# Optimization experiments

Measured on AMD Instinct MI355X. Metric: run time of the kernel, lower is better.

The kernel has to match this reference:

```python
import jax, jax.numpy as jnp
import numpy as np

B, N = 2, 200
IMG = 2048
NC = 4                    # node concepts ('Is*')
NODE_CH = NC * 256        # 1024
EC = 3                    # edge concepts minus 'HigherPri'
AC = 4                    # actions
BBOX_MAX = 1024.0
E = N * (N - 1)

# static fully-connected directed edge list (src=i, dst=j, i!=j), row-major order
_ii, _jj = np.meshgrid(np.arange(N), np.arange(N), indexing='ij')
_m = _ii != _jj
SRC = jnp.asarray(_ii[_m])
DST = jnp.asarray(_jj[_m])


def _lin(k, fin, fout):
    kw, kb = jax.random.split(k)
    s = 1.0 / np.sqrt(fin)
    return (jax.random.uniform(kw, (fin, fout), jnp.float32, -s, s),
            jax.random.uniform(kb, (fout,), jnp.float32, -s, s))


def setup_inputs():
    ks = jax.random.split(jax.random.key(0), 16)
    p = {}
    p['roi_features'] = jax.random.normal(ks[0], (B, N, IMG), jnp.float32)
    p['batch_bboxes'] = jax.random.uniform(ks[1], (B, N, 4), jnp.float32) * BBOX_MAX
    p['batch_directions'] = jax.random.normal(ks[2], (B, N, 4), jnp.float32)
    p['batch_priorities'] = jax.random.normal(ks[3], (B, N), jnp.float32)
    p['w1'], p['b1'] = _lin(ks[4], IMG, 512)
    p['w2'], p['b2'] = _lin(ks[5], 512, 256)
    p['w3'], p['b3'] = _lin(ks[6], 256, NODE_CH)
    p['wi'], p['bi'] = _lin(ks[7], NODE_CH, NC)
    p['we1'], p['be1'] = _lin(ks[8], 16, 256)
    p['we2'], p['be2'] = _lin(ks[9], 256, 64)
    p['we3'], p['be3'] = _lin(ks[10], 64, EC)
    p['wp1'], p['bp1'] = _lin(ks[11], EC + 1, 128)
    p['wp2'], p['bp2'] = _lin(ks[12], 128, NODE_CH * AC)
    p['root_w'], _ = _lin(ks[13], NODE_CH, AC)
    _, p['root_b'] = _lin(ks[14], NODE_CH, AC)
    return p


def reference(roi_features, batch_bboxes, batch_directions, batch_priorities,
              w1, b1, w2, b2, w3, b3, wi, bi,
              we1, be1, we2, be2, we3, be3,
              wp1, bp1, wp2, bp2, root_w, root_b):
    # node concept embedding MLP: [B,N,IMG] -> [B,N,NODE_CH]
    h = jax.nn.relu(roi_features @ w1 + b1)
    h = jax.nn.relu(h @ w2 + b2)
    node_concepts = h @ w3 + b3
    node_concepts_explicit = jax.nn.sigmoid(node_concepts @ wi + bi)

    # pairwise attributes for all directed edges (same ordering as torch masks)
    node_attr = jnp.concatenate([batch_bboxes / BBOX_MAX, batch_directions], -1)  # [B,N,8]
    pair = jnp.concatenate([node_attr[:, SRC], node_attr[:, DST]], -1)            # [B,E,16]
    eh = jax.nn.relu(pair @ we1 + be1)
    eh = jax.nn.relu(eh @ we2 + be2)
    edge_attributes = jax.nn.sigmoid(eh @ we3 + be3)                              # [B,E,EC]
    higher_pri = (batch_priorities[:, SRC] > batch_priorities[:, DST]).astype(jnp.float32)
    edge_attributes = jnp.concatenate([edge_attributes, higher_pri[..., None]], -1)  # [B,E,EC+1]

    # NNConv on graph 0: per-edge weight matrix, gather-matmul-scatter
    x = node_concepts[0]                 # [N, NODE_CH]
    e = edge_attributes[0]               # [E, EC+1]
    w = jax.nn.relu(e @ wp1 + bp1) @ wp2 + bp2
    w = w.reshape(E, NODE_CH, AC)        # [E, NODE_CH, AC]
    msg = jnp.einsum('ei,eio->eo', x[SRC], w)          # [E, AC]
    agg = jax.ops.segment_sum(msg, DST, num_segments=N)  # [N, AC]
    next_actions = agg + x @ root_w + root_b
    return (next_actions, node_concepts_explicit[0], edge_attributes[0])
```

## Files before the change

kernel.cpp:

```cpp
#include <hip/hip_runtime.h>
#include <math.h>

#define NN 200
#define ETOT 39800

typedef float float4v __attribute__((ext_vector_type(4)));
typedef short short8 __attribute__((ext_vector_type(8)));
typedef unsigned int uint4v __attribute__((ext_vector_type(4)));

__device__ __forceinline__ float sigf(float x) { return 1.0f / (1.0f + expf(-x)); }

__device__ __forceinline__ unsigned short f2b(float f) {
  unsigned u = __float_as_uint(f);
  u += 0x7fffu + ((u >> 16) & 1u);
  return (unsigned short)(u >> 16);
}
__device__ __forceinline__ unsigned pk2(float a, float b) {
  unsigned r;
  asm("v_cvt_pk_bf16_f32 %0, %1, %2" : "=v"(r) : "v"(a), "v"(b));
  return r;
}
__device__ __forceinline__ float4v mfma16(short8 a, short8 b, float4v c) {
  return __builtin_amdgcn_mfma_f32_16x16x32_bf16(a, b, c, 0, 0, 0);
}

union SharedU {
  float trans[64][65];
  float red[4][16][34];
  struct { int src_s[64]; int dst_s[64]; } e;
};

template <int KSTEPS>
__device__ __forceinline__ float tile_core(const unsigned short* __restrict__ A,
                                           const unsigned short* __restrict__ B,
                                           int m0, int n0, int K, float (&red)[4][16][34]) {
  const int tid = threadIdx.x, lane = tid & 63, wv = tid >> 6;
  const int mr = lane & 15, quad = lane >> 4;
  const unsigned short* Ap = A + (size_t)(m0 + mr) * K + wv * (KSTEPS * 32) + quad * 8;
  const unsigned short* Bp = B + (size_t)(n0 + mr) * K + wv * (KSTEPS * 32) + quad * 8;
  float4v acc0 = {0.f, 0.f, 0.f, 0.f}, acc1 = {0.f, 0.f, 0.f, 0.f};
#pragma unroll
  for (int s = 0; s < KSTEPS; s += 2) {
    acc0 = mfma16(*(const short8*)(Ap + s * 32), *(const short8*)(Bp + s * 32), acc0);
    acc1 = mfma16(*(const short8*)(Ap + (s + 1) * 32), *(const short8*)(Bp + (s + 1) * 32), acc1);
  }
  float4v acc = acc0 + acc1;
#pragma unroll
  for (int r = 0; r < 4; ++r) red[wv][quad * 4 + r][mr] = acc[r];
  __syncthreads();
  const int row = tid >> 4, col = tid & 15;
  return red[0][row][col] + red[1][row][col] + red[2][row][col] + red[3][row][col];
}

template <int KSTEPS>
__device__ __forceinline__ void tile_core2(const unsigned short* __restrict__ A,
                                           const unsigned short* __restrict__ B,
                                           int m0, int n0, int K,
                                           float& v0, float& v1, float (&red)[4][16][34]) {
  const int tid = threadIdx.x, lane = tid & 63, wv = tid >> 6;
  const int mr = lane & 15, quad = lane >> 4;
  const unsigned short* Ap = A + (size_t)(m0 + mr) * K + wv * (KSTEPS * 32) + quad * 8;
  const unsigned short* B0 = B + (size_t)(n0 + mr) * K + wv * (KSTEPS * 32) + quad * 8;
  const unsigned short* B1 = B0 + (size_t)16 * K;
  float4v a0 = {0.f, 0.f, 0.f, 0.f}, a1 = {0.f, 0.f, 0.f, 0.f};
#pragma unroll
  for (int s = 0; s < KSTEPS; ++s) {
    short8 af = *(const short8*)(Ap + s * 32);
    a0 = mfma16(af, *(const short8*)(B0 + s * 32), a0);
    a1 = mfma16(af, *(const short8*)(B1 + s * 32), a1);
  }
#pragma unroll
  for (int r = 0; r < 4; ++r) {
    red[wv][quad * 4 + r][mr] = a0[r];
    red[wv][quad * 4 + r][17 + mr] = a1[r];
  }
  __syncthreads();
  const int row = tid >> 4, col = tid & 15;
  v0 = red[0][row][col] + red[1][row][col] + red[2][row][col] + red[3][row][col];
  v1 = red[0][row][17 + col] + red[1][row][17 + col] + red[2][row][17 + col] + red[3][row][17 + col];
}

__global__ __launch_bounds__(256) void k_prep(
    const float* __restrict__ w1, const float* __restrict__ roi,
    const float* __restrict__ bbox, const float* __restrict__ dir,
    const float* __restrict__ we1, const float* __restrict__ be1,
    const float* __restrict__ we2,
    unsigned short* __restrict__ w1T, unsigned short* __restrict__ roiB,
    float* __restrict__ P, float* __restrict__ Q, unsigned short* __restrict__ we2T) {
  __shared__ float lds[64][65];
  const int b = blockIdx.x, tid = threadIdx.x;
  if (b < 256) {
    const int kt = b % 32, nt = b / 32;
#pragma unroll 4
    for (int i = 0; i < 16; ++i) {
      int idx = tid + i * 256, r = idx >> 6, c = idx & 63;
      lds[r][c] = w1[(size_t)(kt * 64 + r) * 512 + nt * 64 + c];
    }
    __syncthreads();
#pragma unroll 4
    for (int i = 0; i < 16; ++i) {
      int idx = tid + i * 256, r = idx >> 6, c = idx & 63;
      w1T[(size_t)(nt * 64 + r) * 2048 + kt * 64 + c] = f2b(lds[c][r]);
    }
  } else if (b < 456) {
    int n = b - 256;
    const float4v* R4 = (const float4v*)(roi + (size_t)n * 2048);
    unsigned long long* O = (unsigned long long*)(roiB + (size_t)n * 2048);
#pragma unroll
    for (int j = 0; j < 2; ++j) {
      int idx = tid + j * 256;
      float4v v = R4[idx];
      union { unsigned u[2]; unsigned long long ll; } pk;
      pk.u[0] = pk2(v[0], v[1]);
      pk.u[1] = pk2(v[2], v[3]);
      O[idx] = pk.ll;
    }
  } else if (b < 656) {
    int n = b - 456, c = tid;
    float aa[8];
#pragma unroll
    for (int r = 0; r < 4; ++r) aa[r] = bbox[n * 4 + r] * (1.0f / 1024.0f);
#pragma unroll
    for (int r = 0; r < 4; ++r) aa[4 + r] = dir[n * 4 + r];
    float p = be1[c], q = 0.0f;
#pragma unroll
    for (int r = 0; r < 8; ++r) {
      p += aa[r] * we1[r * 256 + c];
      q += aa[r] * we1[(8 + r) * 256 + c];
    }
    P[n * 256 + c] = p;
    Q[n * 256 + c] = q;
  } else {
    int f = (b - 656) * 256 + tid;
    int c = f >> 6, k0 = (f & 63) * 4;
#pragma unroll
    for (int q = 0; q < 4; ++q)
      we2T[c * 256 + k0 + q] = f2b(we2[(k0 + q) * 64 + c]);
  }
}

__global__ __launch_bounds__(256) void k_g1x(
    const unsigned short* __restrict__ roiB, const unsigned short* __restrict__ w1T,
    const float* __restrict__ b1, unsigned short* __restrict__ h1,
    const float* __restrict__ P, const float* __restrict__ Q,
    const unsigned short* __restrict__ we2T,
    const float* __restrict__ be2, const float* __restrict__ we3, const float* __restrict__ be3,
    const float* __restrict__ pri, float* __restrict__ out_ea,
    const float* __restrict__ w2, unsigned short* __restrict__ w2T,
    const float* __restrict__ wp2, const float* __restrict__ wi,
    const float* __restrict__ rootw, const float* __restrict__ bp2,
    unsigned short* __restrict__ Ac,
    const float* __restrict__ w3, const float* __restrict__ b3, unsigned short* __restrict__ Bc,
    const float* __restrict__ wp1, float* __restrict__ wp1T) {
  __shared__ SharedU sh;
  const int t = blockIdx.x, tid = threadIdx.x;
  if (t < 416) {
    const int m0 = (t % 13) * 16, n0 = (t / 13) * 16;
    float v = tile_core<16>(roiB, w1T, m0, n0, 2048, sh.red);
    const int row = tid >> 4, col = tid & 15;
    v += b1[n0 + col];
    v = fmaxf(v, 0.f);
    h1[(size_t)(m0 + row) * 512 + n0 + col] = f2b(v);
  } else if (t < 1038) {
    const int e0 = (t - 416) * 64;
    if (tid < 64) {
      int e = e0 + tid;
      int i = -1, j = 0;
      if (e < ETOT) {
        i = e / 199;
        int jj = e - i * 199;
        j = jj + (jj >= i ? 1 : 0);
      }
      sh.e.src_s[tid] = i;
      sh.e.dst_s[tid] = j;
    }
    __syncthreads();

    const int lane = tid & 63;
    const int wv = tid >> 6;
    const int m = lane & 15;
    const int quad = lane >> 4;
    const int eloc = wv * 16 + m;
    const int si = sh.e.src_s[eloc];
    const int dj = sh.e.dst_s[eloc];

    float4v acc[4];
#pragma unroll
    for (int ct = 0; ct < 4; ++ct) { acc[ct][0] = 0.f; acc[ct][1] = 0.f; acc[ct][2] = 0.f; acc[ct][3] = 0.f; }

    const short8* W8 = (const short8*)we2T;

    for (int ks = 0; ks < 8; ++ks) {
      union { short8 s; uint4v u; } af;
      af.s = (short8)0;
      if (si >= 0) {
        const float4v* p4 = (const float4v*)(P + si * 256 + ks * 32 + quad * 8);
        const float4v* q4 = (const float4v*)(Q + dj * 256 + ks * 32 + quad * 8);
        float4v v0 = p4[0] + q4[0];
        float4v v1 = p4[1] + q4[1];
        af.u[0] = pk2(fmaxf(v0[0], 0.f), fmaxf(v0[1], 0.f));
        af.u[1] = pk2(fmaxf(v0[2], 0.f), fmaxf(v0[3], 0.f));
        af.u[2] = pk2(fmaxf(v1[0], 0.f), fmaxf(v1[1], 0.f));
        af.u[3] = pk2(fmaxf(v1[2], 0.f), fmaxf(v1[3], 0.f));
      }
#pragma unroll
      for (int ct = 0; ct < 4; ++ct) {
        short8 bf = W8[(ct * 16 + m) * 32 + ks * 4 + quad];
        acc[ct] = __builtin_amdgcn_mfma_f32_16x16x32_bf16(af.s, bf, acc[ct], 0, 0, 0);
      }
    }

    float ev[4][3];
#pragma unroll
    for (int r = 0; r < 4; ++r) { ev[r][0] = 0.f; ev[r][1] = 0.f; ev[r][2] = 0.f; }
#pragma unroll
    for (int ct = 0; ct < 4; ++ct) {
      const int col = ct * 16 + m;
      const float b2v = be2[col];
      const float w0 = we3[col * 3 + 0], w1v = we3[col * 3 + 1], w2v = we3[col * 3 + 2];
#pragma unroll
      for (int r = 0; r < 4; ++r) {
        float e2 = fmaxf(acc[ct][r] + b2v, 0.f);
        ev[r][0] += e2 * w0;
        ev[r][1] += e2 * w1v;
        ev[r][2] += e2 * w2v;
      }
    }
#pragma unroll
    for (int r = 0; r < 4; ++r)
#pragma unroll
      for (int p = 0; p < 3; ++p) {
        float v = ev[r][p];
        v += __shfl_xor(v, 1, 64);
        v += __shfl_xor(v, 2, 64);
        v += __shfl_xor(v, 4, 64);
        v += __shfl_xor(v, 8, 64);
        ev[r][p] = v;
      }
    if (m == 0) {
#pragma unroll
      for (int r = 0; r < 4; ++r) {
        int el = wv * 16 + quad * 4 + r;
        int ss = sh.e.src_s[el], dd = sh.e.dst_s[el];
        if (ss >= 0) {
          float4v o;
          o[0] = sigf(ev[r][0] + be3[0]);
          o[1] = sigf(ev[r][1] + be3[1]);
          o[2] = sigf(ev[r][2] + be3[2]);
          o[3] = (pri[ss] > pri[dd]) ? 1.0f : 0.0f;
          *(float4v*)(out_ea + (size_t)(e0 + el) * 4) = o;
        }
      }
    }
  } else if (t < 1070) {
    const int tt = t - 1038, kt = tt % 8, nt = tt / 8;
#pragma unroll 4
    for (int i = 0; i < 16; ++i) {
      int idx = tid + i * 256, r = idx >> 6, c = idx & 63;
      sh.trans[r][c] = w2[(size_t)(kt * 64 + r) * 256 + nt * 64 + c];
    }
    __syncthreads();
#pragma unroll 4
    for (int i = 0; i < 16; ++i) {
      int idx = tid + i * 256, r = idx >> 6, c = idx & 63;
      w2T[(size_t)(nt * 64 + r) * 512 + kt * 64 + c] = f2b(sh.trans[c][r]);
    }
  } else if (t < 1198) {
    int k = t - 1070;
    int o = tid >> 6, l = tid & 63;
    const float* src = wp2 + (size_t)k * 4096;
    unsigned short* dst = Ac + (size_t)(k * 4 + o) * 1024;
    for (int i = l; i < 1024; i += 64) dst[i] = f2b(src[i * 4 + o]);
  } else if (t < 1214) {
    int r = t - 1198;
    unsigned short* dst = Ac + (size_t)(512 + r) * 1024;
    const float* src = (r < 4) ? (wi + r) : (r < 8) ? (rootw + (r - 4))
                     : (r < 12) ? (bp2 + (r - 8)) : nullptr;
    for (int i = tid; i < 1024; i += 256)
      dst[i] = src ? f2b(src[i * 4]) : (unsigned short)0;
  } else if (t < 1286) {
    int rb = (t - 1214) * 4;
#pragma unroll
    for (int j = 0; j < 16; ++j) {
      int idx = tid + j * 256;
      int row = rb + (idx >> 10), i = idx & 1023;
      float val = (row < 256) ? w3[(size_t)row * 1024 + i] : (row == 256 ? b3[i] : 0.0f);
      Bc[(size_t)row * 1024 + i] = f2b(val);
    }
  } else {
    if (tid < 128) {
      float4v v = {wp1[tid], wp1[128 + tid], wp1[256 + tid], wp1[384 + tid]};
      ((float4v*)wp1T)[tid] = v;
    }
  }
}

__global__ __launch_bounds__(256) void k_g2x(
    const unsigned short* __restrict__ h1, const unsigned short* __restrict__ w2T,
    const float* __restrict__ b2, unsigned short* __restrict__ h2,
    const unsigned short* __restrict__ Ac, const unsigned short* __restrict__ Bc,
    unsigned short* __restrict__ CT, float* __restrict__ biasT) {
  __shared__ SharedU sh;
  const int t = blockIdx.x, tid = threadIdx.x;
  if (t < 208) {
    const int m0 = (t % 13) * 16, n0 = (t / 13) * 16;
    float v = tile_core<4>(h1, w2T, m0, n0, 512, sh.red);
    const int row = tid >> 4, col = tid & 15;
    v += b2[n0 + col];
    v = fmaxf(v, 0.f);
    h2[(size_t)(m0 + row) * 256 + n0 + col] = f2b(v);
  } else {
    const int u = t - 208, mi = u % 33, nj = u / 33;
    const int m0 = mi * 16, n0 = nj * 32;
    float v0, v1;
    tile_core2<8>(Ac, Bc, m0, n0, 1024, v0, v1, sh.red);
    const int row = tid >> 4, col = tid & 15;
    const int m = m0 + row;
    const int c0 = n0 + col, c1 = n0 + 16 + col;
    if (c0 < 256) CT[(size_t)m * 256 + c0] = f2b(v0);
    else if (c0 == 256) biasT[m] = v0;
    if (c1 < 256) CT[(size_t)m * 256 + c1] = f2b(v1);
  }
}

__global__ __launch_bounds__(256) void k_tfused(const unsigned short* __restrict__ h2,
                                                const unsigned short* __restrict__ CT,
                                                const float* __restrict__ biasT,
                                                const float* __restrict__ bi,
                                                const float* __restrict__ rootb,
                                                float* __restrict__ Tm, float* __restrict__ out1,
                                                float* __restrict__ out0, float* __restrict__ U) {
  __shared__ SharedU sh;
  const int m0 = blockIdx.x * 16, n0 = blockIdx.y * 16, tid = threadIdx.x;
  float v = tile_core<2>(h2, CT, m0, n0, 256, sh.red);
  const int row = tid >> 4, col = tid & 15;
  const int n = m0 + row, c = n0 + col;
  v += biasT[c];
  if (c < 512) {
    Tm[(size_t)n * 512 + c] = v;
  } else if (n < NN) {
    int r = c - 512;
    if (r < 4) out1[n * 4 + r] = sigf(v + bi[r]);
    else if (r < 8) out0[n * 4 + (r - 4)] = v + rootb[r - 4];
    else if (r < 12) U[n * 4 + (r - 8)] = v;
  }
}

__global__ __launch_bounds__(256) void k_tail(
    const float* __restrict__ ea, const float* __restrict__ wp1T, const float* __restrict__ bp1,
    const float* __restrict__ T, const float* __restrict__ U,
    float* __restrict__ out0) {
  __shared__ int src_s[64], dst_s[64];
  __shared__ float4v ea_s[64];
  __shared__ float4v wp1s[128];
  __shared__ float bp1s[128];
  __shared__ float4v Ts[2][128];
  __shared__ float Us[2][4];

  const int tid = threadIdx.x;
  const int e0 = blockIdx.x * 64;
  const int s_lo = e0 / 199;

  if (tid < 64) {
    int e = e0 + tid;
    int i = -1, j = 0;
    if (e < ETOT) {
      i = e / 199;
      int jj = e - i * 199;
      j = jj + (jj >= i ? 1 : 0);
      ea_s[tid] = ((const float4v*)ea)[e];
    }
    src_s[tid] = i;
    dst_s[tid] = j;
  }
  if (tid < 128) {
    wp1s[tid] = ((const float4v*)wp1T)[tid];
    bp1s[tid] = bp1[tid];
  }
  {
    int row = tid >> 7, c = tid & 127;
    Ts[row][c] = ((const float4v*)T)[(s_lo + row) * 128 + c];
  }
  if (tid < 8) {
    int s = min(s_lo + (tid >> 2), 199);
    Us[tid >> 2][tid & 3] = U[s * 4 + (tid & 3)];
  }
  __syncthreads();

  const int ee = tid >> 2, pp = tid & 3;
  const int s2 = src_s[ee], d2 = dst_s[ee];
  float4v pm = {0.f, 0.f, 0.f, 0.f};
  if (s2 >= 0) {
    const int srow = s2 - s_lo;
    const float4v c4 = ea_s[ee];
    const float c0 = c4[0], c1 = c4[1], c2 = c4[2], c3 = c4[3];
#pragma unroll 8
    for (int tt = pp; tt < 128; tt += 4) {
      float4v w4 = wp1s[tt];
      float hv = bp1s[tt] + c0 * w4[0] + c1 * w4[1] + c2 * w4[2] + c3 * w4[3];
      hv = fmaxf(hv, 0.f);
      pm += hv * Ts[srow][tt];
    }
  }
#pragma unroll
  for (int o = 0; o < 4; ++o) {
    float v = pm[o];
    v += __shfl_xor(v, 1, 64);
    v += __shfl_xor(v, 2, 64);
    pm[o] = v;
  }
  if (s2 >= 0) atomicAdd(&out0[d2 * 4 + pp], Us[s2 - s_lo][pp] + pm[pp]);
}

extern "C" void kernel_launch(void* const* d_in, const int* in_sizes, int n_in,
                              void* d_out, int out_size, void* d_ws, size_t ws_size,
                              hipStream_t stream) {
  (void)in_sizes; (void)n_in; (void)out_size; (void)ws_size;
  const float* roi   = (const float*)d_in[0];
  const float* bbox  = (const float*)d_in[1];
  const float* dir   = (const float*)d_in[2];
  const float* pri   = (const float*)d_in[3];
  const float* w1    = (const float*)d_in[4];
  const float* b1    = (const float*)d_in[5];
  const float* w2    = (const float*)d_in[6];
  const float* b2    = (const float*)d_in[7];
  const float* w3    = (const float*)d_in[8];
  const float* b3    = (const float*)d_in[9];
  const float* wi    = (const float*)d_in[10];
  const float* bi    = (const float*)d_in[11];
  const float* we1   = (const float*)d_in[12];
  const float* be1   = (const float*)d_in[13];
  const float* we2   = (const float*)d_in[14];
  const float* be2   = (const float*)d_in[15];
  const float* we3   = (const float*)d_in[16];
  const float* be3   = (const float*)d_in[17];
  const float* wp1   = (const float*)d_in[18];
  const float* bp1   = (const float*)d_in[19];
  const float* wp2   = (const float*)d_in[20];
  const float* bp2   = (const float*)d_in[21];
  const float* rootw = (const float*)d_in[22];
  const float* rootb = (const float*)d_in[23];

  float* out0 = (float*)d_out;
  float* out1 = out0 + 800;
  float* out2 = out0 + 1600;

  unsigned short* us = (unsigned short*)d_ws;
  unsigned short* w1T  = us;
  unsigned short* w2T  = us + 1048576;
  unsigned short* Ac   = us + 1179648;
  unsigned short* Bc   = us + 1720320;
  unsigned short* we2T = us + 2015232;
  unsigned short* roiB = us + 2031616;
  unsigned short* h1   = us + 2457600;
  unsigned short* h2   = us + 2564096;
  unsigned short* CT   = us + 2617344;
  float* fb    = (float*)(us + 2752512);
  float* Tm    = fb;
  float* Pm    = fb + 106496;
  float* Qm    = fb + 157696;
  float* Um    = fb + 208896;
  float* wp1Tp = fb + 209696;
  float* biasT = fb + 210208;

  k_prep<<<672, 256, 0, stream>>>(w1, roi, bbox, dir, we1, be1, we2,
                                  w1T, roiB, Pm, Qm, we2T);

  k_g1x<<<1287, 256, 0, stream>>>(roiB, w1T, b1, h1,
                                  Pm, Qm, we2T, be2, we3, be3, pri, out2,
                                  w2, w2T,
                                  wp2, wi, rootw, bp2, Ac,
                                  w3, b3, Bc,
                                  wp1, wp1Tp);

  k_g2x<<<505, 256, 0, stream>>>(h1, w2T, b2, h2, Ac, Bc, CT, biasT);

  k_tfused<<<dim3(13, 33), 256, 0, stream>>>(h2, CT, biasT, bi, rootb, Tm, out1, out0, Um);

  k_tail<<<622, 256, 0, stream>>>(out2, wp1Tp, bp1, Tm, Um, out0);
}
```

Before: 155.2 us.

## Fuse layer-2 GEMM, transform GEMM and edge tail into per-node final kernel

Moves all weight-conversion work into the prep kernel and runs the Ac·Bc product in the same launch as the layer-1 GEMM and the edge MLP. The layer-2 matmul, the projection through CT and the per-edge message aggregation are merged into one kernel with one block per source node. Each block computes its node's h2 and T rows in LDS with scalar FMAs instead of MFMA, then processes that node's 199 outgoing edges. This cuts the pipeline from five launches to three and removes the global round trips for h2, T and U, at the cost of scalar fp32 math and only 200 blocks in the last stage.

```diff
diff --git a/kernel.cpp b/kernel.cpp
--- a/kernel.cpp
+++ b/kernel.cpp
@@ -15,6 +15,11 @@
   u += 0x7fffu + ((u >> 16) & 1u);
   return (unsigned short)(u >> 16);
 }
+__device__ __forceinline__ float b2f16(unsigned short u) {
+  return __uint_as_float(((unsigned)u) << 16);
+}
+__device__ __forceinline__ float blo(unsigned u) { return __uint_as_float(u << 16); }
+__device__ __forceinline__ float bhi(unsigned u) { return __uint_as_float(u & 0xffff0000u); }
 __device__ __forceinline__ unsigned pk2(float a, float b) {
   unsigned r;
   asm("v_cvt_pk_bf16_f32 %0, %1, %2" : "=v"(r) : "v"(a), "v"(b));
@@ -84,9 +89,15 @@
     const float* __restrict__ w1, const float* __restrict__ roi,
     const float* __restrict__ bbox, const float* __restrict__ dir,
     const float* __restrict__ we1, const float* __restrict__ be1,
-    const float* __restrict__ we2,
+    const float* __restrict__ we2, const float* __restrict__ w2,
+    const float* __restrict__ wp2, const float* __restrict__ wi,
+    const float* __restrict__ rootw, const float* __restrict__ bp2,
+    const float* __restrict__ w3, const float* __restrict__ b3,
+    const float* __restrict__ wp1,
     unsigned short* __restrict__ w1T, unsigned short* __restrict__ roiB,
-    float* __restrict__ P, float* __restrict__ Q, unsigned short* __restrict__ we2T) {
+    float* __restrict__ P, float* __restrict__ Q, unsigned short* __restrict__ we2T,
+    unsigned short* __restrict__ w2T, unsigned short* __restrict__ Ac,
+    unsigned short* __restrict__ Bc, float* __restrict__ wp1T) {
   __shared__ float lds[64][65];
   const int b = blockIdx.x, tid = threadIdx.x;
   if (b < 256) {
@@ -130,28 +141,64 @@
     }
     P[n * 256 + c] = p;
     Q[n * 256 + c] = q;
-  } else {
+  } else if (b < 672) {
     int f = (b - 656) * 256 + tid;
     int c = f >> 6, k0 = (f & 63) * 4;
 #pragma unroll
     for (int q = 0; q < 4; ++q)
       we2T[c * 256 + k0 + q] = f2b(we2[(k0 + q) * 64 + c]);
-  }
-}
-
-__global__ __launch_bounds__(256) void k_g1x(
+  } else if (b < 704) {
+    const int tt = b - 672, kt = tt % 8, nt = tt / 8;
+#pragma unroll 4
+    for (int i = 0; i < 16; ++i) {
+      int idx = tid + i * 256, r = idx >> 6, c = idx & 63;
+      lds[r][c] = w2[(size_t)(kt * 64 + r) * 256 + nt * 64 + c];
+    }
+    __syncthreads();
+#pragma unroll 4
+    for (int i = 0; i < 16; ++i) {
+      int idx = tid + i * 256, r = idx >> 6, c = idx & 63;
+      w2T[(size_t)(nt * 64 + r) * 512 + kt * 64 + c] = f2b(lds[c][r]);
+    }
+  } else if (b < 832) {
+    int k = b - 704;
+    int o = tid >> 6, l = tid & 63;
+    const float* src = wp2 + (size_t)k * 4096;
+    unsigned short* dst = Ac + (size_t)(k * 4 + o) * 1024;
+    for (int i = l; i < 1024; i += 64) dst[i] = f2b(src[i * 4 + o]);
+  } else if (b < 848) {
+    int r = b - 832;
+    unsigned short* dst = Ac + (size_t)(512 + r) * 1024;
+    const float* src = (r < 4) ? (wi + r) : (r < 8) ? (rootw + (r - 4))
+                     : (r < 12) ? (bp2 + (r - 8)) : nullptr;
+    for (int i = tid; i < 1024; i += 256)
+      dst[i] = src ? f2b(src[i * 4]) : (unsigned short)0;
+  } else if (b < 920) {
+    int rb = (b - 848) * 4;
+#pragma unroll
+    for (int j = 0; j < 16; ++j) {
+      int idx = tid + j * 256;
+      int row = rb + (idx >> 10), i = idx & 1023;
+      float val = (row < 256) ? w3[(size_t)row * 1024 + i] : (row == 256 ? b3[i] : 0.0f);
+      Bc[(size_t)row * 1024 + i] = f2b(val);
+    }
+  } else {
+    if (tid < 128) {
+      float4v v = {wp1[tid], wp1[128 + tid], wp1[256 + tid], wp1[384 + tid]};
+      ((float4v*)wp1T)[tid] = v;
+    }
+  }
+}
+
+__global__ __launch_bounds__(256) void k_main(
     const unsigned short* __restrict__ roiB, const unsigned short* __restrict__ w1T,
     const float* __restrict__ b1, unsigned short* __restrict__ h1,
     const float* __restrict__ P, const float* __restrict__ Q,
     const unsigned short* __restrict__ we2T,
     const float* __restrict__ be2, const float* __restrict__ we3, const float* __restrict__ be3,
     const float* __restrict__ pri, float* __restrict__ out_ea,
-    const float* __restrict__ w2, unsigned short* __restrict__ w2T,
-    const float* __restrict__ wp2, const float* __restrict__ wi,
-    const float* __restrict__ rootw, const float* __restrict__ bp2,
-    unsigned short* __restrict__ Ac,
-    const float* __restrict__ w3, const float* __restrict__ b3, unsigned short* __restrict__ Bc,
-    const float* __restrict__ wp1, float* __restrict__ wp1T) {
+    const unsigned short* __restrict__ Ac, const unsigned short* __restrict__ Bc,
+    unsigned short* __restrict__ CT, float* __restrict__ biasT) {
   __shared__ SharedU sh;
   const int t = blockIdx.x, tid = threadIdx.x;
   if (t < 416) {
@@ -252,65 +299,8 @@
         }
       }
     }
-  } else if (t < 1070) {
-    const int tt = t - 1038, kt = tt % 8, nt = tt / 8;
-#pragma unroll 4
-    for (int i = 0; i < 16; ++i) {
-      int idx = tid + i * 256, r = idx >> 6, c = idx & 63;
-      sh.trans[r][c] = w2[(size_t)(kt * 64 + r) * 256 + nt * 64 + c];
-    }
-    __syncthreads();
-#pragma unroll 4
-    for (int i = 0; i < 16; ++i) {
-      int idx = tid + i * 256, r = idx >> 6, c = idx & 63;
-      w2T[(size_t)(nt * 64 + r) * 512 + kt * 64 + c] = f2b(sh.trans[c][r]);
-    }
-  } else if (t < 1198) {
-    int k = t - 1070;
-    int o = tid >> 6, l = tid & 63;
-    const float* src = wp2 + (size_t)k * 4096;
-    unsigned short* dst = Ac + (size_t)(k * 4 + o) * 1024;
-    for (int i = l; i < 1024; i += 64) dst[i] = f2b(src[i * 4 + o]);
-  } else if (t < 1214) {
-    int r = t - 1198;
-    unsigned short* dst = Ac + (size_t)(512 + r) * 1024;
-    const float* src = (r < 4) ? (wi + r) : (r < 8) ? (rootw + (r - 4))
-                     : (r < 12) ? (bp2 + (r - 8)) : nullptr;
-    for (int i = tid; i < 1024; i += 256)
-      dst[i] = src ? f2b(src[i * 4]) : (unsigned short)0;
-  } else if (t < 1286) {
-    int rb = (t - 1214) * 4;
-#pragma unroll
-    for (int j = 0; j < 16; ++j) {
-      int idx = tid + j * 256;
-      int row = rb + (idx >> 10), i = idx & 1023;
-      float val = (row < 256) ? w3[(size_t)row * 1024 + i] : (row == 256 ? b3[i] : 0.0f);
-      Bc[(size_t)row * 1024 + i] = f2b(val);
-    }
   } else {
-    if (tid < 128) {
-      float4v v = {wp1[tid], wp1[128 + tid], wp1[256 + tid], wp1[384 + tid]};
-      ((float4v*)wp1T)[tid] = v;
-    }
-  }
-}
-
-__global__ __launch_bounds__(256) void k_g2x(
-    const unsigned short* __restrict__ h1, const unsigned short* __restrict__ w2T,
-    const float* __restrict__ b2, unsigned short* __restrict__ h2,
-    const unsigned short* __restrict__ Ac, const unsigned short* __restrict__ Bc,
-    unsigned short* __restrict__ CT, float* __restrict__ biasT) {
-  __shared__ SharedU sh;
-  const int t = blockIdx.x, tid = threadIdx.x;
-  if (t < 208) {
-    const int m0 = (t % 13) * 16, n0 = (t / 13) * 16;
-    float v = tile_core<4>(h1, w2T, m0, n0, 512, sh.red);
-    const int row = tid >> 4, col = tid & 15;
-    v += b2[n0 + col];
-    v = fmaxf(v, 0.f);
-    h2[(size_t)(m0 + row) * 256 + n0 + col] = f2b(v);
-  } else {
-    const int u = t - 208, mi = u % 33, nj = u / 33;
+    const int u = t - 1038, mi = u % 33, nj = u / 33;
     const int m0 = mi * 16, n0 = nj * 32;
     float v0, v1;
     tile_core2<8>(Ac, Bc, m0, n0, 1024, v0, v1, sh.red);
@@ -323,93 +313,100 @@
   }
 }
 
-__global__ __launch_bounds__(256) void k_tfused(const unsigned short* __restrict__ h2,
-                                                const unsigned short* __restrict__ CT,
-                                                const float* __restrict__ biasT,
-                                                const float* __restrict__ bi,
-                                                const float* __restrict__ rootb,
-                                                float* __restrict__ Tm, float* __restrict__ out1,
-                                                float* __restrict__ out0, float* __restrict__ U) {
-  __shared__ SharedU sh;
-  const int m0 = blockIdx.x * 16, n0 = blockIdx.y * 16, tid = threadIdx.x;
-  float v = tile_core<2>(h2, CT, m0, n0, 256, sh.red);
-  const int row = tid >> 4, col = tid & 15;
-  const int n = m0 + row, c = n0 + col;
-  v += biasT[c];
-  if (c < 512) {
-    Tm[(size_t)n * 512 + c] = v;
-  } else if (n < NN) {
-    int r = c - 512;
-    if (r < 4) out1[n * 4 + r] = sigf(v + bi[r]);
-    else if (r < 8) out0[n * 4 + (r - 4)] = v + rootb[r - 4];
-    else if (r < 12) U[n * 4 + (r - 8)] = v;
-  }
-}
-
-__global__ __launch_bounds__(256) void k_tail(
-    const float* __restrict__ ea, const float* __restrict__ wp1T, const float* __restrict__ bp1,
-    const float* __restrict__ T, const float* __restrict__ U,
-    float* __restrict__ out0) {
-  __shared__ int src_s[64], dst_s[64];
-  __shared__ float4v ea_s[64];
+__global__ __launch_bounds__(256) void k_final(
+    const unsigned short* __restrict__ h1, const unsigned short* __restrict__ w2T,
+    const float* __restrict__ b2,
+    const unsigned short* __restrict__ CT, const float* __restrict__ biasT,
+    const float* __restrict__ bi, const float* __restrict__ rootb,
+    const float* __restrict__ ea,
+    const float* __restrict__ wp1T, const float* __restrict__ bp1,
+    float* __restrict__ out0, float* __restrict__ out1) {
+  __shared__ float h1s[512];
+  __shared__ float h2f[256];
+  __shared__ float4v Ts4[128];
   __shared__ float4v wp1s[128];
   __shared__ float bp1s[128];
-  __shared__ float4v Ts[2][128];
-  __shared__ float Us[2][4];
-
-  const int tid = threadIdx.x;
-  const int e0 = blockIdx.x * 64;
-  const int s_lo = e0 / 199;
-
-  if (tid < 64) {
-    int e = e0 + tid;
-    int i = -1, j = 0;
-    if (e < ETOT) {
-      i = e / 199;
-      int jj = e - i * 199;
-      j = jj + (jj >= i ? 1 : 0);
-      ea_s[tid] = ((const float4v*)ea)[e];
-    }
-    src_s[tid] = i;
-    dst_s[tid] = j;
+  __shared__ float Us[4];
+  const int s = blockIdx.x, tid = threadIdx.x;
+
+  {
+    unsigned u = ((const unsigned*)(h1 + (size_t)s * 512))[tid];
+    h1s[2 * tid] = blo(u);
+    h1s[2 * tid + 1] = bhi(u);
   }
   if (tid < 128) {
     wp1s[tid] = ((const float4v*)wp1T)[tid];
     bp1s[tid] = bp1[tid];
   }
+  __syncthreads();
+
   {
-    int row = tid >> 7, c = tid & 127;
-    Ts[row][c] = ((const float4v*)T)[(s_lo + row) * 128 + c];
-  }
-  if (tid < 8) {
-    int s = min(s_lo + (tid >> 2), 199);
-    Us[tid >> 2][tid & 3] = U[s * 4 + (tid & 3)];
+    const uint4v* W4 = (const uint4v*)(w2T + (size_t)tid * 512);
+    float acc = b2[tid];
+#pragma unroll 8
+    for (int j = 0; j < 64; ++j) {
+      uint4v w = W4[j];
+      const float4v* hp = (const float4v*)&h1s[j * 8];
+      float4v ha = hp[0], hb = hp[1];
+      acc += ha[0] * blo(w[0]) + ha[1] * bhi(w[0]) + ha[2] * blo(w[1]) + ha[3] * bhi(w[1]) +
+             hb[0] * blo(w[2]) + hb[1] * bhi(w[2]) + hb[2] * blo(w[3]) + hb[3] * bhi(w[3]);
+    }
+    h2f[tid] = fmaxf(acc, 0.f);
   }
   __syncthreads();
 
-  const int ee = tid >> 2, pp = tid & 3;
-  const int s2 = src_s[ee], d2 = dst_s[ee];
-  float4v pm = {0.f, 0.f, 0.f, 0.f};
-  if (s2 >= 0) {
-    const int srow = s2 - s_lo;
-    const float4v c4 = ea_s[ee];
-    const float c0 = c4[0], c1 = c4[1], c2 = c4[2], c3 = c4[3];
+#pragma unroll
+  for (int rr = 0; rr < 2; ++rr) {
+    int c = 2 * tid + rr;
+    const uint4v* C4 = (const uint4v*)(CT + (size_t)c * 256);
+    float acc = biasT[c];
 #pragma unroll 8
-    for (int tt = pp; tt < 128; tt += 4) {
-      float4v w4 = wp1s[tt];
-      float hv = bp1s[tt] + c0 * w4[0] + c1 * w4[1] + c2 * w4[2] + c3 * w4[3];
-      hv = fmaxf(hv, 0.f);
-      pm += hv * Ts[srow][tt];
-    }
-  }
-#pragma unroll
-  for (int o = 0; o < 4; ++o) {
-    float v = pm[o];
-    v += __shfl_xor(v, 1, 64);
-    v += __shfl_xor(v, 2, 64);
-    pm[o] = v;
-  }
-  if (s2 >= 0) atomicAdd(&out0[d2 * 4 + pp], Us[s2 - s_lo][pp] + pm[pp]);
+    for (int j = 0; j < 32; ++j) {
+      uint4v w = C4[j];
+      const float4v* hp = (const float4v*)&h2f[j * 8];
+      float4v ha = hp[0], hb = hp[1];
+      acc += ha[0] * blo(w[0]) + ha[1] * bhi(w[0]) + ha[2] * blo(w[1]) + ha[3] * bhi(w[1]) +
+             hb[0] * blo(w[2]) + hb[1] * bhi(w[2]) + hb[2] * blo(w[3]) + hb[3] * bhi(w[3]);
+    }
+    ((float*)Ts4)[c] = acc;
+  }
+  if (tid < 12) {
+    int c = 512 + tid;
+    const uint4v* C4 = (const uint4v*)(CT + (size_t)c * 256);
+    float acc = biasT[c];
+#pragma unroll 8
+    for (int j = 0; j < 32; ++j) {
+      uint4v w = C4[j];
+      const float4v* hp = (const float4v*)&h2f[j * 8];
+      float4v ha = hp[0], hb = hp[1];
+      acc += ha[0] * blo(w[0]) + ha[1] * bhi(w[0]) + ha[2] * blo(w[1]) + ha[3] * bhi(w[1]) +
+             hb[0] * blo(w[2]) + hb[1] * bhi(w[2]) + hb[2] * blo(w[3]) + hb[3] * bhi(w[3]);
+    }
+    if (tid < 4) out1[s * 4 + tid] = sigf(acc + bi[tid]);
+    else if (tid < 8) atomicAdd(&out0[s * 4 + (tid - 4)], acc + rootb[tid - 4]);
+    else Us[tid - 8] = acc;
+  }
+  __syncthreads();
+
+  if (tid < 199) {
+    const int d = tid + (tid >= s ? 1 : 0);
+    const float4v c4 = ((const float4v*)ea)[s * 199 + tid];
+    float m0 = 0.f, m1 = 0.f, m2 = 0.f, m3 = 0.f;
+#pragma unroll 8
+    for (int k = 0; k < 128; ++k) {
+      float4v w4 = wp1s[k];
+      float hv = fmaxf(bp1s[k] + c4[0] * w4[0] + c4[1] * w4[1] + c4[2] * w4[2] + c4[3] * w4[3], 0.f);
+      float4v t4 = Ts4[k];
+      m0 += hv * t4[0];
+      m1 += hv * t4[1];
+      m2 += hv * t4[2];
+      m3 += hv * t4[3];
+    }
+    atomicAdd(&out0[d * 4 + 0], Us[0] + m0);
+    atomicAdd(&out0[d * 4 + 1], Us[1] + m1);
+    atomicAdd(&out0[d * 4 + 2], Us[2] + m2);
+    atomicAdd(&out0[d * 4 + 3], Us[3] + m3);
+  }
 }
 
 extern "C" void kernel_launch(void* const* d_in, const int* in_sizes, int n_in,
@@ -453,29 +450,21 @@
   unsigned short* we2T = us + 2015232;
   unsigned short* roiB = us + 2031616;
   unsigned short* h1   = us + 2457600;
-  unsigned short* h2   = us + 2564096;
   unsigned short* CT   = us + 2617344;
   float* fb    = (float*)(us + 2752512);
-  float* Tm    = fb;
   float* Pm    = fb + 106496;
   float* Qm    = fb + 157696;
-  float* Um    = fb + 208896;
   float* wp1Tp = fb + 209696;
   float* biasT = fb + 210208;
 
-  k_prep<<<672, 256, 0, stream>>>(w1, roi, bbox, dir, we1, be1, we2,
-                                  w1T, roiB, Pm, Qm, we2T);
-
-  k_g1x<<<1287, 256, 0, stream>>>(roiB, w1T, b1, h1,
-                                  Pm, Qm, we2T, be2, we3, be3, pri, out2,
-                                  w2, w2T,
-                                  wp2, wi, rootw, bp2, Ac,
-                                  w3, b3, Bc,
-                                  wp1, wp1Tp);
-
-  k_g2x<<<505, 256, 0, stream>>>(h1, w2T, b2, h2, Ac, Bc, CT, biasT);
-
-  k_tfused<<<dim3(13, 33), 256, 0, stream>>>(h2, CT, biasT, bi, rootb, Tm, out1, out0, Um);
-
-  k_tail<<<622, 256, 0, stream>>>(out2, wp1Tp, bp1, Tm, Um, out0);
-}
+  k_prep<<<921, 256, 0, stream>>>(w1, roi, bbox, dir, we1, be1, we2, w2,
+                                  wp2, wi, rootw, bp2, w3, b3, wp1,
+                                  w1T, roiB, Pm, Qm, we2T, w2T, Ac, Bc, wp1Tp);
+
+  k_main<<<1335, 256, 0, stream>>>(roiB, w1T, b1, h1,
+                                   Pm, Qm, we2T, be2, we3, be3, pri, out2,
+                                   Ac, Bc, CT, biasT);
+
+  k_final<<<200, 256, 0, stream>>>(h1, w2T, b2, CT, biasT, bi, rootb,
+                                   out2, wp1Tp, bp1, out0, out1);
+}
```

Result: slower. 191.9 us (+23.6%).
